# Performance work log

Measured on AMD Instinct MI355X. Metric: run time of the kernel, lower is better.

The kernel has to match this reference:

```python
import jax, jax.numpy as jnp
import numpy as np

N_SAMPLES = 32768; WINDOW = 512; STEP = 256; N_FRAMES = 128
N_COEFFS = 257; N_ATOMS = 32; MODEL_DIM = 128
DILATIONS = (1, 3, 9, 27, 81, 243, 1)


def _conv1d(x, w, b=None, dilation=1, padding=0):
    o = jax.lax.conv_general_dilated(x, w, (1,), [(padding, padding)],
                                     rhs_dilation=(dilation,),
                                     dimension_numbers=('NCH', 'OIH', 'NCH'))
    return o if b is None else o + b[None, :, None]


def _leaky(x):
    return jnp.where(x >= 0, x, 0.2 * x)


def _lin_stack(x, ws, bs, ow, ob):
    # LinearOutputStack: hidden linears with leaky relu, final linear
    for i in range(ws.shape[0]):
        x = _leaky(x @ ws[i].T + bs[i])
    return x @ ow.T + ob


def _conv_up(z, lw, lb, cw, cb, fw, fb_):
    x = (z @ lw.T + lb).reshape(-1, MODEL_DIM, 8)
    for i in range(cw.shape[0]):
        x = jnp.repeat(x, 2, axis=-1)
        x = _leaky(_conv1d(x, cw[i], cb[i], padding=1))
    return _conv1d(x, fw, fb_, padding=1)


def _lin_upsample(x, out_len):
    # F.upsample(mode='linear', align_corners=False)
    L = x.shape[-1]
    src = jnp.clip((jnp.arange(out_len) + 0.5) * (L / out_len) - 0.5, 0.0, L - 1)
    i0 = jnp.floor(src).astype(jnp.int32)
    i1 = jnp.minimum(i0 + 1, L - 1)
    t = (src - i0).astype(x.dtype)
    return x[..., i0] * (1 - t) + x[..., i1] * t


def _generate_event(envelope, transfer, impulse_tf, impulse_noise):
    # envelope [N,1,S], transfer [N,257,2,128], impulse_tf [N,257,2]
    tf = jax.lax.complex(transfer[:, :, 0, :], transfer[:, :, 1, :])  # [N,257,128]
    itf = jax.lax.complex(impulse_tf[..., 0], impulse_tf[..., 1])     # [N,257]
    spec = jnp.fft.rfft(impulse_noise, norm='ortho') * itf
    impulse = jnp.fft.irfft(spec, n=WINDOW, norm='ortho')             # [N,512]
    env = jnp.pad(envelope[:, 0, :], ((0, 0), (0, STEP)))             # pad last frame
    win_idx = (jnp.arange(N_FRAMES) * STEP)[:, None] + jnp.arange(WINDOW)  # [128,512]
    env_frames = env[:, win_idx]                                      # [N,128,512]
    ham = (0.54 - 0.46 * jnp.cos(2 * jnp.pi * jnp.arange(WINDOW) / WINDOW)).astype(envelope.dtype)

    def step(carry, inp):
        env_f, tf_f = inp                      # [N,512], [N,257]
        nxt = impulse * env_f + carry
        s = jnp.fft.rfft(nxt, norm='ortho') * tf_f
        out = jnp.fft.irfft(s, n=WINDOW, norm='ortho') * ham
        return out, out

    _, frames = jax.lax.scan(step, jnp.zeros_like(impulse),
                             (env_frames.transpose(1, 0, 2), tf.transpose(2, 0, 1)))
    frames = frames.transpose(1, 0, 2)         # [N,128,512]
    buf = jnp.zeros((frames.shape[0], N_FRAMES * STEP + STEP), frames.dtype)
    buf = buf.at[:, win_idx].add(frames)       # overlap-add, hop 256
    return buf[:, :N_SAMPLES]


def reference(x, fb_w,
              db_scale_w, db_scale_b, db_gate_w, db_gate_b,
              db_out_w, db_out_b, db_next_w, db_next_b,
              env_lin_w, env_lin_b, env_conv_w, env_conv_b, env_fin_w, env_fin_b,
              tf_lin_w, tf_lin_b, tf_conv_w, tf_conv_b, tf_fin_w, tf_fin_b,
              imp_w, imp_b, imp_out_w, imp_out_b,
              room_w, room_b, room_out_w, room_out_b,
              mix_w, mix_b, mix_out_w, mix_out_b,
              rooms, impulse_noise):
    B = x.shape[0]
    # FilterBank: conv over raw audio, same length
    n = jax.lax.conv_general_dilated(x, fb_w, (1,), [(256, 255)],
                                     dimension_numbers=('NCH', 'OIH', 'NCH'))  # [B,128,S]
    acc = jnp.zeros_like(n)
    for i, d in enumerate(DILATIONS):
        skip = n
        s = _conv1d(n, db_scale_w[i], db_scale_b[i], dilation=d, padding=d)
        g = _conv1d(n, db_gate_w[i], db_gate_b[i], dilation=d, padding=d)
        h = jnp.tanh(s) * jax.nn.sigmoid(g)
        acc = acc + jnp.einsum('oc,bct->bot', db_out_w[i], h) + db_out_b[i][None, :, None]
        n = jnp.einsum('oc,bct->bot', db_next_w[i], h) + db_next_b[i][None, :, None] + skip
    xf = acc                                                   # [B,128,S]
    norms = jnp.linalg.norm(xf, axis=1)                        # [B,S]
    values, indices = jax.lax.top_k(norms, N_ATOMS)            # [B,32]
    latents = jnp.take_along_axis(xf, indices[:, None, :], axis=2)  # [B,128,32]
    latents = latents.transpose(0, 2, 1).reshape(B * N_ATOMS, MODEL_DIM)
    # EventGenerator
    env = _conv_up(latents, env_lin_w, env_lin_b, env_conv_w, env_conv_b, env_fin_w, env_fin_b) ** 2
    env = _lin_upsample(env, N_SAMPLES)                        # [N,1,S]
    transfer = _conv_up(latents, tf_lin_w, tf_lin_b, tf_conv_w, tf_conv_b, tf_fin_w, tf_fin_b)
    transfer = transfer.reshape(-1, N_COEFFS, 2, N_FRAMES)
    impulse_tf = _lin_stack(latents, imp_w, imp_b, imp_out_w, imp_out_b).reshape(-1, N_COEFFS, 2)
    atoms = _generate_event(env, transfer, impulse_tf, impulse_noise).reshape(B, N_ATOMS, N_SAMPLES)
    # scatter-add atoms at topk offsets into 2*S buffer
    pos = indices[:, :, None] + jnp.arange(N_SAMPLES)[None, None, :]   # [B,32,S]
    weighted = atoms * values[:, :, None]

    def scat(pos_b, w_b):
        return jnp.zeros(2 * N_SAMPLES, w_b.dtype).at[pos_b.reshape(-1)].add(w_b.reshape(-1))

    final = jax.vmap(scat)(pos, weighted)[:, None, :N_SAMPLES]         # [B,1,S]
    # reverb mix
    agg = jnp.max(xf, axis=-1)                                         # [B,128]
    r = _lin_stack(agg, room_w, room_b, room_out_w, room_out_b)        # [B,n_rooms]
    m = _lin_stack(agg, mix_w, mix_b, mix_out_w, mix_out_b).reshape(-1, 1, 1)
    ir = jax.nn.softmax(r, axis=-1) @ rooms                            # [B,S]
    fs = jnp.fft.rfft(final[:, 0, :], n=2 * N_SAMPLES)
    irs = jnp.fft.rfft(ir, n=2 * N_SAMPLES)
    wet = jnp.fft.irfft(fs * irs, n=2 * N_SAMPLES)[:, None, :N_SAMPLES]
    return m * wet + final * (1 - m)


def setup_inputs() -> dict:
    key = jax.random.key(0)
    ks = iter(jax.random.split(key, 64))

    def w(*shape, s=0.05):
        return jax.random.normal(next(ks), shape, dtype=jnp.float32) * s

    return {
        'x': jax.random.normal(next(ks), (4, 1, N_SAMPLES), dtype=jnp.float32),
        'fb_w': w(128, 1, 512),
        'db_scale_w': w(7, 128, 128, 3), 'db_scale_b': w(7, 128),
        'db_gate_w': w(7, 128, 128, 3), 'db_gate_b': w(7, 128),
        'db_out_w': w(7, 128, 128), 'db_out_b': w(7, 128),
        'db_next_w': w(7, 128, 128), 'db_next_b': w(7, 128),
        'env_lin_w': w(1024, 128), 'env_lin_b': w(1024),
        'env_conv_w': w(4, 128, 128, 3), 'env_conv_b': w(4, 128),
        'env_fin_w': w(1, 128, 3), 'env_fin_b': w(1),
        'tf_lin_w': w(1024, 128), 'tf_lin_b': w(1024),
        'tf_conv_w': w(4, 128, 128, 3), 'tf_conv_b': w(4, 128),
        'tf_fin_w': w(514, 128, 3), 'tf_fin_b': w(514),
        'imp_w': w(3, 128, 128), 'imp_b': w(3, 128),
        'imp_out_w': w(514, 128), 'imp_out_b': w(514),
        'room_w': w(3, 128, 128), 'room_b': w(3, 128),
        'room_out_w': w(8, 128), 'room_out_b': w(8),
        'mix_w': w(3, 128, 128), 'mix_b': w(3, 128),
        'mix_out_w': w(1, 128), 'mix_out_b': w(1),
        'rooms': w(8, N_SAMPLES, s=0.1),
        'impulse_noise': jax.random.uniform(next(ks), (1, WINDOW), minval=-1.0, maxval=1.0, dtype=jnp.float32),
    }
```

## Files before the change

### kernel.cpp

```cpp
#include <hip/hip_runtime.h>
#include <math.h>

#define NS 32768

static __device__ __forceinline__ float leakyf(float x){ return x >= 0.f ? x : 0.2f*x; }

__global__ void k_wtrans(const float* __restrict__ ws, const float* __restrict__ wg, float* __restrict__ wT)
{
    int idx = blockIdx.x*256 + threadIdx.x;
    const int total = 7*2*3*128*128;
    if (idx >= total) return;
    int o  = idx & 127;
    int cc = (idx >> 7) & 127;
    int j  = (idx >> 14) % 3;
    int sg = (idx / 49152) & 1;
    int l  = idx / 98304;
    const float* src = sg ? wg : ws;
    wT[idx] = src[((l*128 + o)*128 + cc)*3 + j];
}

__global__ void k_wtrans2(const float* __restrict__ wo, const float* __restrict__ wn,
                          float* __restrict__ woT, float* __restrict__ wnT)
{
    int idx = blockIdx.x*256 + threadIdx.x;
    if (idx >= 7*128*128) return;
    int o = idx & 127;
    int c = (idx >> 7) & 127;
    int l = idx >> 14;
    woT[idx] = wo[(l*128 + o)*128 + c];
    wnT[idx] = wn[(l*128 + o)*128 + c];
}

__global__ void k_wtrans_up(const float* __restrict__ ecw, const float* __restrict__ tcw,
                            const float* __restrict__ tfw, float* __restrict__ wtu, float* __restrict__ wtf)
{
    int idx = blockIdx.x*256 + threadIdx.x;
    if (idx < 393216) {
        int o = idx & 127;
        int j = (idx >> 7) % 3;
        int c = (idx / 384) & 127;
        int ml = idx / 49152;
        const float* src = (ml < 4 ? ecw : tcw) + (ml & 3)*49152;
        wtu[idx] = src[(o*128 + c)*3 + j];
    }
    if (idx < 208896) {
        int ct = idx % 544;
        int j = (idx / 544) % 3;
        int c = idx / 1632;
        wtf[idx] = (ct < 514) ? tfw[(ct*128 + c)*3 + j] : 0.f;
    }
}

__global__ __launch_bounds__(512) void k_front(const float* __restrict__ x, const float* __restrict__ fbw,
                                               float* __restrict__ n0)
{
    int b = blockIdx.y;
    int t0 = blockIdx.x * 64;
    int tid = threadIdx.x;
    int t = tid & 63, og = tid >> 6;
    __shared__ float xs[576];
    __shared__ float4 wl[2048];
    for (int i = tid; i < 575; i += 512) {
        int p = t0 + i - 256;
        xs[i] = ((unsigned)p < NS) ? x[b*NS + p] : 0.f;
    }
    float s[16];
    #pragma unroll
    for (int i = 0; i < 16; ++i) s[i] = 0.f;
    for (int kc = 0; kc < 8; ++kc) {
        __syncthreads();
        for (int i = tid; i < 2048; i += 512) {
            int c = i >> 4, k4 = i & 15;
            wl[i] = *(const float4*)(fbw + c*512 + kc*64 + k4*4);
        }
        __syncthreads();
        for (int k4 = 0; k4 < 16; ++k4) {
            int base = t + kc*64 + k4*4;
            float xv0 = xs[base+0], xv1 = xs[base+1], xv2 = xs[base+2], xv3 = xs[base+3];
            #pragma unroll
            for (int i = 0; i < 16; ++i) {
                float4 w = wl[(og*16 + i)*16 + k4];
                s[i] += w.x*xv0 + w.y*xv1 + w.z*xv2 + w.w*xv3;
            }
        }
    }
    #pragma unroll
    for (int i = 0; i < 16; ++i)
        n0[(size_t)(b*128 + og*16 + i)*NS + t0 + t] = s[i];
}

__global__ __launch_bounds__(512) void k_layer(const float* __restrict__ nin, float* __restrict__ nout,
        float* __restrict__ acc, const float* __restrict__ wTl,
        const float* __restrict__ bs, const float* __restrict__ bg,
        const float* __restrict__ woTl, const float* __restrict__ bo,
        const float* __restrict__ wnTl, const float* __restrict__ bn,
        int d, int first)
{
    __shared__ float pool[20480];
    int b = blockIdx.y;
    int t0 = blockIdx.x * 128;
    int tid = threadIdx.x;
    int l = tid & 63, wg = tid >> 6;
    int o0 = wg * 16;
    const float* nb = nin + (size_t)b*128*NS;
    const float4* wq = (const float4*)wTl;

    int sci = tid >> 5;
    int st4 = (tid & 31) * 4;
    int wsgA = 0,              wccA = (tid >> 5) & 15,        wo4A = tid & 31;
    int wsgB = (tid+512) >> 9, wccB = ((tid+512) >> 5) & 15,  wo4B = (tid+512) & 31;

    float4 sreg, wr0, wr1;
    {
        int p = t0 + st4 - d;
        const float* bp = nb + (size_t)sci*NS;
        float v0 = ((unsigned)(p+0) < NS) ? bp[p+0] : 0.f;
        float v1 = ((unsigned)(p+1) < NS) ? bp[p+1] : 0.f;
        float v2 = ((unsigned)(p+2) < NS) ? bp[p+2] : 0.f;
        float v3 = ((unsigned)(p+3) < NS) ? bp[p+3] : 0.f;
        sreg = make_float4(v0,v1,v2,v3);
        wr0 = wq[((wsgA*3 + 0)*128 + wccA)*32 + wo4A];
        wr1 = wq[((wsgB*3 + 0)*128 + wccB)*32 + wo4B];
    }

    float s0[16], s1[16], g0[16], g1[16];
    #pragma unroll
    for (int i = 0; i < 16; ++i) { float bv = bs[o0+i], gv = bg[o0+i]; s0[i]=bv; s1[i]=bv; g0[i]=gv; g1[i]=gv; }

    #pragma unroll 1
    for (int cnt = 0; cnt < 24; ++cnt) {
        int cur = cnt & 1;
        ((float4*)(pool + cur*2048))[tid] = sreg;
        {
            float4* wb = (float4*)(pool + 4096 + cur*4096);
            wb[tid] = wr0; wb[tid + 512] = wr1;
        }
        if (cnt < 23) {
            int nxt = cnt + 1;
            int jn = nxt >> 3, cbn = nxt & 7;
            int p = t0 + st4 + (jn-1)*d;
            const float* bp = nb + (size_t)(cbn*16 + sci)*NS;
            float v0 = ((unsigned)(p+0) < NS) ? bp[p+0] : 0.f;
            float v1 = ((unsigned)(p+1) < NS) ? bp[p+1] : 0.f;
            float v2 = ((unsigned)(p+2) < NS) ? bp[p+2] : 0.f;
            float v3 = ((unsigned)(p+3) < NS) ? bp[p+3] : 0.f;
            sreg = make_float4(v0,v1,v2,v3);
            wr0 = wq[((wsgA*3 + jn)*128 + cbn*16 + wccA)*32 + wo4A];
            wr1 = wq[((wsgB*3 + jn)*128 + cbn*16 + wccB)*32 + wo4B];
        }
        __syncthreads();
        const float* sb = pool + cur*2048;
        const float4* wS = (const float4*)(pool + 4096 + cur*4096);
        const float4* wG = wS + 512;
        for (int ccx = 0; ccx < 16; ++ccx) {
            float nv0 = sb[ccx*128 + l];
            float nv1 = sb[ccx*128 + 64 + l];
            const float4* a4p = wS + ccx*32 + wg*4;
            const float4* b4p = wG + ccx*32 + wg*4;
            #pragma unroll
            for (int i4 = 0; i4 < 4; ++i4) {
                float4 a4 = a4p[i4], b4 = b4p[i4];
                s0[i4*4+0] += nv0*a4.x; s0[i4*4+1] += nv0*a4.y; s0[i4*4+2] += nv0*a4.z; s0[i4*4+3] += nv0*a4.w;
                s1[i4*4+0] += nv1*a4.x; s1[i4*4+1] += nv1*a4.y; s1[i4*4+2] += nv1*a4.z; s1[i4*4+3] += nv1*a4.w;
                g0[i4*4+0] += nv0*b4.x; g0[i4*4+1] += nv0*b4.y; g0[i4*4+2] += nv0*b4.z; g0[i4*4+3] += nv0*b4.w;
                g1[i4*4+0] += nv1*b4.x; g1[i4*4+1] += nv1*b4.y; g1[i4*4+2] += nv1*b4.z; g1[i4*4+3] += nv1*b4.w;
            }
        }
    }

    float hv0[16], hv1[16];
    #pragma unroll
    for (int i = 0; i < 16; ++i) {
        hv0[i] = tanhf(s0[i]) * (1.f/(1.f + __expf(-g0[i])));
        hv1[i] = tanhf(s1[i]) * (1.f/(1.f + __expf(-g1[i])));
    }
    __syncthreads();
    #pragma unroll
    for (int i = 0; i < 16; ++i) {
        pool[(o0+i)*128 + l]      = hv0[i];
        pool[(o0+i)*128 + 64 + l] = hv1[i];
    }

    int aarm = tid >> 8, arest = tid & 255;
    int accx = arest >> 5, ao4 = arest & 31;
    float4 w2r;
    {
        const float4* src = (const float4*)(aarm ? wnTl : woTl);
        w2r = src[(0*8 + accx)*32 + ao4];
    }

    float a0[16], a1[16], n0r[16], n1r[16];
    #pragma unroll
    for (int i = 0; i < 16; ++i) { a0[i]=0.f; a1[i]=0.f; n0r[i]=0.f; n1r[i]=0.f; }

    #pragma unroll 1
    for (int cb2 = 0; cb2 < 16; ++cb2) {
        int cur = cb2 & 1;
        ((float4*)(pool + 16384 + cur*2048))[tid] = w2r;
        if (cb2 < 15) {
            const float4* src = (const float4*)(aarm ? wnTl : woTl);
            w2r = src[((cb2+1)*8 + accx)*32 + ao4];
        }
        __syncthreads();
        const float4* w2S = (const float4*)(pool + 16384 + cur*2048);
        const float4* w2N = w2S + 256;
        for (int ccx = 0; ccx < 8; ++ccx) {
            float h0 = pool[(cb2*8 + ccx)*128 + l];
            float h1 = pool[(cb2*8 + ccx)*128 + 64 + l];
            const float4* wo4p = w2S + ccx*32 + wg*4;
            const float4* wn4p = w2N + ccx*32 + wg*4;
            #pragma unroll
            for (int i4 = 0; i4 < 4; ++i4) {
                float4 w0 = wo4p[i4], w1 = wn4p[i4];
                a0[i4*4+0] += h0*w0.x; a0[i4*4+1] += h0*w0.y; a0[i4*4+2] += h0*w0.z; a0[i4*4+3] += h0*w0.w;
                a1[i4*4+0] += h1*w0.x; a1[i4*4+1] += h1*w0.y; a1[i4*4+2] += h1*w0.z; a1[i4*4+3] += h1*w0.w;
                n0r[i4*4+0] += h0*w1.x; n0r[i4*4+1] += h0*w1.y; n0r[i4*4+2] += h0*w1.z; n0r[i4*4+3] += h0*w1.w;
                n1r[i4*4+0] += h1*w1.x; n1r[i4*4+1] += h1*w1.y; n1r[i4*4+2] += h1*w1.z; n1r[i4*4+3] += h1*w1.w;
            }
        }
    }

    #pragma unroll
    for (int i = 0; i < 16; ++i) {
        int o = o0 + i;
        float bov = bo[o], bnv = bn[o];
        size_t gi0 = (size_t)(b*128 + o)*NS + t0 + l;
        size_t gi1 = gi0 + 64;
        float av0 = first ? 0.f : acc[gi0];
        float av1 = first ? 0.f : acc[gi1];
        acc[gi0] = av0 + a0[i] + bov;
        acc[gi1] = av1 + a1[i] + bov;
        nout[gi0] = n0r[i] + bnv + nin[gi0];
        nout[gi1] = n1r[i] + bnv + nin[gi1];
    }
}

__global__ void k_norms(const float* __restrict__ xf, float* __restrict__ norms)
{
    int b = blockIdx.y;
    int t = blockIdx.x*256 + threadIdx.x;
    float a = 0.f;
    for (int c = 0; c < 128; ++c) {
        float v = xf[(size_t)(b*128 + c)*NS + t];
        a += v*v;
    }
    norms[b*NS + t] = a;
}

__global__ __launch_bounds__(1024) void k_topk(float* __restrict__ norms, float* __restrict__ topv, int* __restrict__ topi)
{
    int b = blockIdx.x;
    int tid = threadIdx.x;
    __shared__ float rv[1024];
    __shared__ int   ri[1024];
    for (int it = 0; it < 32; ++it) {
        float best = -2.f; int bi = 0;
        for (int k = tid; k < NS; k += 1024) {
            float v = norms[b*NS + k];
            if (v > best) { best = v; bi = k; }
        }
        rv[tid] = best; ri[tid] = bi;
        __syncthreads();
        for (int off = 512; off > 0; off >>= 1) {
            if (tid < off) {
                float ov = rv[tid+off]; int oi = ri[tid+off];
                if (ov > rv[tid] || (ov == rv[tid] && oi < ri[tid])) { rv[tid] = ov; ri[tid] = oi; }
            }
            __syncthreads();
        }
        if (tid == 0) {
            topv[b*32 + it] = sqrtf(rv[0]);
            topi[b*32 + it] = ri[0];
            norms[b*NS + ri[0]] = -1.f;
        }
        __syncthreads();
    }
}

__global__ void k_latents(const float* __restrict__ xf, const int* __restrict__ topi, float* __restrict__ lat)
{
    int ev = blockIdx.x; int c = threadIdx.x;
    int b = ev >> 5;
    int idx = topi[ev];
    lat[ev*128 + c] = xf[(size_t)(b*128 + c)*NS + idx];
}

__global__ void k_aggmax(const float* __restrict__ xf, float* __restrict__ agg)
{
    int rc = blockIdx.x;
    int tid = threadIdx.x;
    __shared__ float red[256];
    float m = -3.4e38f;
    const float* row = xf + (size_t)rc*NS;
    for (int t = tid; t < NS; t += 256) m = fmaxf(m, row[t]);
    red[tid] = m; __syncthreads();
    for (int off = 128; off > 0; off >>= 1) {
        if (tid < off) red[tid] = fmaxf(red[tid], red[tid+off]);
        __syncthreads();
    }
    if (tid == 0) agg[rc] = red[0];
}

template<int L2, int NPASS>
__device__ __forceinline__ void up_layerS(const float* __restrict__ wbase, const float* __restrict__ bias,
                                          const float* __restrict__ inb, float* __restrict__ outb,
                                          float* __restrict__ wst, int tid)
{
    constexpr int Lin = L2/2;
    constexpr int OGC = 512/L2;
    constexpr int OR  = 128/NPASS;
    constexpr int NO  = OR/OGC;
    constexpr int LOG = (L2==16)?4:(L2==32)?5:(L2==64)?6:7;
    int p  = tid & (L2-1);
    int og = tid >> LOG;
    int o0 = og*NO;
    #pragma unroll 1
    for (int pass = 0; pass < NPASS; ++pass) {
        int obase = pass*OR;
        float acc[NO];
        #pragma unroll
        for (int k = 0; k < NO; ++k) acc[k] = 0.f;
        #pragma unroll 1
        for (int cc0 = 0; cc0 < 128; cc0 += 16) {
            __syncthreads();
            for (int k = tid; k < 16*3*OR; k += 512) {
                int ci = k / (3*OR); int rem = k - ci*(3*OR);
                int j = rem / OR; int oo = rem - j*OR;
                wst[k] = wbase[(cc0+ci)*384 + j*128 + obase + oo];
            }
            __syncthreads();
            #pragma unroll 1
            for (int ci = 0; ci < 16; ++ci) {
                int c = cc0 + ci;
                float xv[3];
                #pragma unroll
                for (int j = 0; j < 3; ++j) {
                    int iu = p + j - 1;
                    xv[j] = ((unsigned)iu < (unsigned)L2) ? inb[c*Lin + (iu>>1)] : 0.f;
                }
                #pragma unroll
                for (int j = 0; j < 3; ++j) {
                    const float4* w4 = (const float4*)(wst + ci*3*OR + j*OR + o0);
                    #pragma unroll
                    for (int q = 0; q < NO/4; ++q) {
                        float4 w = w4[q];
                        acc[q*4+0] += xv[j]*w.x; acc[q*4+1] += xv[j]*w.y;
                        acc[q*4+2] += xv[j]*w.z; acc[q*4+3] += xv[j]*w.w;
                    }
                }
            }
        }
        #pragma unroll
        for (int k = 0; k < NO; ++k)
            outb[(obase + o0 + k)*L2 + p] = leakyf(acc[k] + bias[obase + o0 + k]);
    }
}

__global__ __launch_bounds__(512) void k_convup3(const float* __restrict__ lat,
    const float* __restrict__ elw, const float* __restrict__ elb, const float* __restrict__ ecb,
    const float* __restrict__ efw, const float* __restrict__ efb,
    const float* __restrict__ tlw, const float* __restrict__ tlb, const float* __restrict__ tcb,
    const float* __restrict__ tfb, const float* __restrict__ wtu, const float* __restrict__ wtf,
    float* __restrict__ envsq, float* __restrict__ tfT)
{
    __shared__ float pool[35008];
    float* latv = pool;
    float* bufA = pool + 128;
    float* bufB = pool + 4288;
    float* bufC = pool + 12480;
    float* wst  = pool + 28864;
    int ev = blockIdx.x;
    int m  = blockIdx.y;
    int tid = threadIdx.x;
    const float* lw = m ? tlw : elw;
    const float* lb = m ? tlb : elb;
    const float* cb = m ? tcb : ecb;
    const float* wu = wtu + m*4*49152;
    if (tid < 128) latv[tid] = lat[ev*128 + tid];
    __syncthreads();
    for (int jj = tid; jj < 1024; jj += 512) {
        float a = lb[jj];
        const float4* w4 = (const float4*)(lw + jj*128);
        #pragma unroll 8
        for (int q = 0; q < 32; ++q) {
            float4 w = w4[q];
            a += w.x*latv[q*4] + w.y*latv[q*4+1] + w.z*latv[q*4+2] + w.w*latv[q*4+3];
        }
        bufA[(jj>>3)*8 + (jj&7)] = a;
    }
    up_layerS<16,1>(wu,        cb,     bufA, bufB, wst, tid);
    up_layerS<32,1>(wu+49152,  cb+128, bufB, bufA, wst, tid);
    up_layerS<64,2>(wu+98304,  cb+256, bufA, bufB, wst, tid);
    up_layerS<128,4>(wu+147456,cb+384, bufB, bufC, wst, tid);
    __syncthreads();
    int p = tid & 127, g = tid >> 7;
    if (m == 0) {
        float s = 0.f;
        #pragma unroll 1
        for (int c = g*32; c < g*32+32; ++c) {
            #pragma unroll
            for (int j = 0; j < 3; ++j) {
                int iu = p + j - 1;
                float xv = ((unsigned)iu < 128u) ? bufC[c*128 + iu] : 0.f;
                s += efw[c*3+j]*xv;
            }
        }
        wst[g*128 + p] = s;
        __syncthreads();
        if (g == 0) {
            float a = wst[p] + wst[128+p] + wst[256+p] + wst[384+p] + efb[0];
            envsq[ev*128 + p] = a*a;
        }
    } else {
        float* trb = bufA;
        #pragma unroll 1
        for (int ctb = 0; ctb < 17; ++ctb) {
            int ct0 = ctb*32;
            float acc[8];
            #pragma unroll
            for (int i = 0; i < 8; ++i) acc[i] = 0.f;
            #pragma unroll 1
            for (int cc0 = 0; cc0 < 128; cc0 += 16) {
                __syncthreads();
                for (int k = tid; k < 1536; k += 512) {
                    int ci = k / 96, rem = k - ci*96;
                    int j = rem >> 5, ctl = rem & 31;
                    wst[k] = wtf[(cc0+ci)*1632 + j*544 + ct0 + ctl];
                }
                __syncthreads();
                #pragma unroll 1
                for (int ci = 0; ci < 16; ++ci) {
                    int c = cc0 + ci;
                    float xv[3];
                    #pragma unroll
                    for (int j = 0; j < 3; ++j) {
                        int iu = p + j - 1;
                        xv[j] = ((unsigned)iu < 128u) ? bufC[c*128 + iu] : 0.f;
                    }
                    #pragma unroll
                    for (int j = 0; j < 3; ++j) {
                        const float4* w4 = (const float4*)(wst + ci*96 + j*32 + g*8);
                        #pragma unroll
                        for (int q = 0; q < 2; ++q) {
                            float4 w = w4[q];
                            acc[q*4+0] += xv[j]*w.x; acc[q*4+1] += xv[j]*w.y;
                            acc[q*4+2] += xv[j]*w.z; acc[q*4+3] += xv[j]*w.w;
                        }
                    }
                }
            }
            __syncthreads();
            #pragma unroll
            for (int i = 0; i < 8; ++i) trb[(g*8 + i)*129 + p] = acc[i];
            __syncthreads();
            int ctl2 = tid & 31, pg = tid >> 5;
            #pragma unroll 1
            for (int ps = 0; ps < 8; ++ps) {
                int pp = ps*16 + pg;
                int ct = ct0 + ctl2;
                if (ct < 514)
                    tfT[(size_t)(ev*128 + pp)*514 + ct] = trb[ctl2*129 + pp] + tfb[ct];
            }
            __syncthreads();
        }
    }
}

__global__ __launch_bounds__(128) void k_itf(const float* __restrict__ lat,
    const float* __restrict__ iw, const float* __restrict__ ib,
    const float* __restrict__ iow, const float* __restrict__ iob,
    float* __restrict__ itf)
{
    int ev = blockIdx.x; int tid = threadIdx.x;
    __shared__ float xa[128], xb[128];
    xa[tid] = lat[ev*128 + tid];
    __syncthreads();
    float* src = xa; float* dst = xb;
    for (int l = 0; l < 3; ++l) {
        float a = ib[l*128 + tid];
        const float* wr = iw + (l*128 + tid)*128;
        for (int k = 0; k < 128; ++k) a += wr[k]*src[k];
        dst[tid] = leakyf(a);
        __syncthreads();
        float* tmp = src; src = dst; dst = tmp;
    }
    for (int o = tid; o < 514; o += 128) {
        float a = iob[o];
        const float* wr = iow + o*128;
        for (int k = 0; k < 128; ++k) a += wr[k]*src[k];
        itf[ev*514 + o] = a;
    }
}

__global__ __launch_bounds__(128) void k_roommix(const float* __restrict__ agg,
    const float* __restrict__ rw, const float* __restrict__ rb,
    const float* __restrict__ row_, const float* __restrict__ rob,
    const float* __restrict__ mw, const float* __restrict__ mb,
    const float* __restrict__ mow, const float* __restrict__ mob,
    float* __restrict__ probs, float* __restrict__ mval)
{
    int b = blockIdx.x; int tid = threadIdx.x;
    __shared__ float xa[128], xb[128], rr[8];
    xa[tid] = agg[b*128 + tid];
    __syncthreads();
    float* src = xa; float* dst = xb;
    for (int l = 0; l < 3; ++l) {
        float a = rb[l*128 + tid];
        const float* wr = rw + (l*128 + tid)*128;
        for (int k = 0; k < 128; ++k) a += wr[k]*src[k];
        dst[tid] = leakyf(a);
        __syncthreads();
        float* tmp = src; src = dst; dst = tmp;
    }
    if (tid < 8) {
        float a = rob[tid];
        const float* wr = row_ + tid*128;
        for (int k = 0; k < 128; ++k) a += wr[k]*src[k];
        rr[tid] = a;
    }
    __syncthreads();
    if (tid == 0) {
        float m = rr[0];
        for (int j = 1; j < 8; ++j) m = fmaxf(m, rr[j]);
        float ssum = 0.f; float e[8];
        for (int j = 0; j < 8; ++j) { e[j] = __expf(rr[j]-m); ssum += e[j]; }
        for (int j = 0; j < 8; ++j) probs[b*8+j] = e[j]/ssum;
    }
    __syncthreads();
    xa[tid] = agg[b*128 + tid];
    __syncthreads();
    src = xa; dst = xb;
    for (int l = 0; l < 3; ++l) {
        float a = mb[l*128 + tid];
        const float* wr = mw + (l*128 + tid)*128;
        for (int k = 0; k < 128; ++k) a += wr[k]*src[k];
        dst[tid] = leakyf(a);
        __syncthreads();
        float* tmp = src; src = dst; dst = tmp;
    }
    if (tid == 0) {
        float a = mob[0];
        for (int k = 0; k < 128; ++k) a += mow[k]*src[k];
        mval[b] = a;
    }
}

__global__ void k_ir(const float* __restrict__ probs, const float* __restrict__ rooms, float* __restrict__ ir)
{
    int b = blockIdx.y;
    int t = blockIdx.x*256 + threadIdx.x;
    float a = 0.f;
    for (int j = 0; j < 8; ++j) a += probs[b*8+j]*rooms[j*NS + t];
    ir[b*NS + t] = a;
}

__device__ __forceinline__ void fft512(float* re, float* im, const float* twr, const float* twi, int tid, bool inverse)
{
    for (int w = tid; w < 512; w += 256) {
        unsigned r = __brev((unsigned)w) >> 23;
        if ((int)r > w) {
            float tr = re[w]; re[w] = re[r]; re[r] = tr;
            float ti = im[w]; im[w] = im[r]; im[r] = ti;
        }
    }
    __syncthreads();
    for (int s = 0; s < 9; ++s) {
        int half = 1 << s;
        int grp = tid >> s;
        int pos = tid & (half-1);
        int i0 = (grp << (s+1)) + pos;
        int i1 = i0 + half;
        int twidx = pos << (8 - s);
        float wr = twr[twidx];
        float wi = inverse ? -twi[twidx] : twi[twidx];
        float r1 = re[i1], q1 = im[i1];
        float tr = wr*r1 - wi*q1;
        float ti = wr*q1 + wi*r1;
        float r0 = re[i0], q0 = im[i0];
        re[i1] = r0 - tr; im[i1] = q0 - ti;
        re[i0] = r0 + tr; im[i0] = q0 + ti;
        __syncthreads();
    }
}

__global__ __launch_bounds__(256) void k_event(const float* __restrict__ tfT, const float* __restrict__ itf,
    const float* __restrict__ envsq, const float* __restrict__ noise, float* __restrict__ atoms)
{
    int ev = blockIdx.x; int tid = threadIdx.x;
    __shared__ float twr[256], twi[256];
    __shared__ float re[512], im[512], carry[512], imp[512], ham[512], acc[256], envl[128];
    if (tid < 128) envl[tid] = envsq[ev*128 + tid];
    {
        float ang = -6.283185307179586f * (float)tid / 512.0f;
        float si, co;
        sincosf(ang, &si, &co);
        twr[tid] = co; twi[tid] = si;
    }
    for (int w = tid; w < 512; w += 256) {
        ham[w] = 0.54f - 0.46f*cosf(6.283185307179586f * (float)w / 512.0f);
        re[w] = noise[w]; im[w] = 0.f; carry[w] = 0.f;
    }
    acc[tid] = 0.f;
    __syncthreads();
    fft512(re, im, twr, twi, tid, false);
    {
        const float* tp = itf + ev*514;
        int k = tid;
        float xr = re[k], xi = im[k];
        float tr = tp[2*k], ti = tp[2*k+1];
        float sr = xr*tr - xi*ti;
        float si = xr*ti + xi*tr;
        if (k == 0) si = 0.f;
        re[k] = sr; im[k] = si;
        if (k >= 1) { re[512-k] = sr; im[512-k] = -si; }
        if (tid == 0) {
            float xr2 = re[256], xi2 = im[256];
            float sr2 = xr2*tp[512] - xi2*tp[513];
            re[256] = sr2; im[256] = 0.f;
        }
    }
    __syncthreads();
    fft512(re, im, twr, twi, tid, true);
    for (int w = tid; w < 512; w += 256) imp[w] = re[w] * (1.0f/512.0f);
    __syncthreads();
    const float inv512 = 1.0f/512.0f;
    for (int f = 0; f < 128; ++f) {
        for (int w = tid; w < 512; w += 256) {
            int tg = f*256 + w;
            float e = 0.f;
            if (tg < NS) {
                float srcp = ((float)tg + 0.5f)*(1.0f/256.0f) - 0.5f;
                srcp = fminf(fmaxf(srcp, 0.f), 127.f);
                int i0 = (int)srcp;
                float fr = srcp - (float)i0;
                int i1 = i0 + 1; if (i1 > 127) i1 = 127;
                e = envl[i0]*(1.f-fr) + envl[i1]*fr;
            }
            re[w] = imp[w]*e + carry[w];
            im[w] = 0.f;
        }
        __syncthreads();
        fft512(re, im, twr, twi, tid, false);
        {
            const float* tp = tfT + ((size_t)ev*128 + f)*514;
            int k = tid;
            float xr = re[k], xi = im[k];
            float tr = tp[2*k], ti = tp[2*k+1];
            float sr = xr*tr - xi*ti;
            float si = xr*ti + xi*tr;
            if (k == 0) si = 0.f;
            re[k] = sr; im[k] = si;
            if (k >= 1) { re[512-k] = sr; im[512-k] = -si; }
            if (tid == 0) {
                float xr2 = re[256], xi2 = im[256];
                float sr2 = xr2*tp[512] - xi2*tp[513];
                re[256] = sr2; im[256] = 0.f;
            }
        }
        __syncthreads();
        fft512(re, im, twr, twi, tid, true);
        float o0 = re[tid]     * inv512 * ham[tid];
        float o1 = re[tid+256] * inv512 * ham[tid+256];
        atoms[(size_t)ev*NS + f*256 + tid] = o0 + acc[tid];
        acc[tid] = o1;
        carry[tid] = o0;
        carry[tid+256] = o1;
        __syncthreads();
    }
}

__global__ void k_gather(const float* __restrict__ atoms, const float* __restrict__ topv,
                         const int* __restrict__ topi, float* __restrict__ fin)
{
    int b = blockIdx.y;
    int t = blockIdx.x*256 + threadIdx.x;
    float s = 0.f;
    for (int a = 0; a < 32; ++a) {
        int ii = topi[b*32 + a];
        if (ii <= t) s += topv[b*32 + a] * atoms[(size_t)(b*32 + a)*NS + (t - ii)];
    }
    fin[b*NS + t] = s;
}

__global__ __launch_bounds__(256) void k_wetpart(const float* __restrict__ fin, const float* __restrict__ ir,
                                                 float* __restrict__ wetp)
{
    int t0 = blockIdx.x*256;
    int by = blockIdx.y;
    int b = by >> 3, cg = by & 7;
    int tid = threadIdx.x;
    __shared__ float fs[256];
    __shared__ float irw[512];
    float wet = 0.f;
    int nch = t0/256 + 1;
    #pragma unroll 1
    for (int q = cg; q < nch; q += 8) {
        int c0 = q*256;
        __syncthreads();
        fs[tid] = fin[b*NS + c0 + tid];
        int dmin = t0 - c0 - 255;
        for (int qq = tid; qq < 511; qq += 256) {
            int dd = dmin + qq;
            irw[qq] = ((unsigned)dd < NS) ? ir[b*NS + dd] : 0.f;
        }
        __syncthreads();
        if (c0 < t0) {
            #pragma unroll 8
            for (int k = 0; k < 256; ++k) wet += fs[k]*irw[tid + 255 - k];
        } else {
            for (int k = 0; k <= tid; ++k) wet += fs[k]*irw[tid + 255 - k];
        }
    }
    wetp[(size_t)by*NS + t0 + tid] = wet;
}

__global__ __launch_bounds__(256) void k_wetsum(const float* __restrict__ fin, const float* __restrict__ wetp,
                                                const float* __restrict__ mval, float* __restrict__ out)
{
    int b = blockIdx.y;
    int t = blockIdx.x*256 + threadIdx.x;
    float w = 0.f;
    #pragma unroll
    for (int cg = 0; cg < 8; ++cg) w += wetp[(size_t)(b*8+cg)*NS + t];
    float m = mval[b];
    float fv = fin[b*NS + t];
    out[b*NS + t] = m*w + fv*(1.f - m);
}

extern "C" void kernel_launch(void* const* d_in, const int* in_sizes, int n_in,
                              void* d_out, int out_size, void* d_ws, size_t ws_size,
                              hipStream_t stream)
{
    (void)in_sizes; (void)n_in; (void)out_size; (void)ws_size;
    const float* x    = (const float*)d_in[0];
    const float* fbw  = (const float*)d_in[1];
    const float* dsw  = (const float*)d_in[2];
    const float* dsb  = (const float*)d_in[3];
    const float* dgw  = (const float*)d_in[4];
    const float* dgb  = (const float*)d_in[5];
    const float* dow  = (const float*)d_in[6];
    const float* dob  = (const float*)d_in[7];
    const float* dnw  = (const float*)d_in[8];
    const float* dnb  = (const float*)d_in[9];
    const float* elw  = (const float*)d_in[10];
    const float* elb  = (const float*)d_in[11];
    const float* ecw  = (const float*)d_in[12];
    const float* ecb  = (const float*)d_in[13];
    const float* efw  = (const float*)d_in[14];
    const float* efb  = (const float*)d_in[15];
    const float* tlw  = (const float*)d_in[16];
    const float* tlb  = (const float*)d_in[17];
    const float* tcw  = (const float*)d_in[18];
    const float* tcb  = (const float*)d_in[19];
    const float* tfw  = (const float*)d_in[20];
    const float* tfb  = (const float*)d_in[21];
    const float* iw   = (const float*)d_in[22];
    const float* ib   = (const float*)d_in[23];
    const float* iow  = (const float*)d_in[24];
    const float* iob  = (const float*)d_in[25];
    const float* rw   = (const float*)d_in[26];
    const float* rb   = (const float*)d_in[27];
    const float* row_ = (const float*)d_in[28];
    const float* rob  = (const float*)d_in[29];
    const float* mw   = (const float*)d_in[30];
    const float* mb   = (const float*)d_in[31];
    const float* mow  = (const float*)d_in[32];
    const float* mob  = (const float*)d_in[33];
    const float* rooms= (const float*)d_in[34];
    const float* noise= (const float*)d_in[35];

    float* ws   = (float*)d_ws;
    float* n0   = ws;
    float* n1   = ws + 16777216;
    float* accb = ws + 33554432;
    float* wT   = ws + 50331648;
    float* woT  = ws + 51707904;
    float* wnT  = ws + 51822592;
    float* envsq= ws + 51937280;
    float* lat  = ws + 51953664;
    float* itfb = ws + 51970048;
    float* norms= ws + 52035840;
    float* topv = ws + 52166912;
    int*   topi = (int*)(ws + 52167040);
    float* agg  = ws + 52167168;
    float* probs= ws + 52167680;
    float* mval = ws + 52167712;
    float* irb  = ws + 52167744;
    float* fin  = ws + 52298816;
    float* tfT  = n0;
    float* atoms= n0 + 8421376;
    float* wetp = n0 + 12615680;
    float* wtu  = n1;
    float* wtf  = n1 + 393216;

    float* out = (float*)d_out;

    k_wtrans<<<dim3((1376256+255)/256), dim3(256), 0, stream>>>(dsw, dgw, wT);
    k_wtrans2<<<dim3((114688+255)/256), dim3(256), 0, stream>>>(dow, dnw, woT, wnT);
    k_front<<<dim3(512,4), dim3(512), 0, stream>>>(x, fbw, n0);

    const int dil[7] = {1,3,9,27,81,243,1};
    float* cin = n0; float* cout = n1;
    for (int l = 0; l < 7; ++l) {
        k_layer<<<dim3(256,4), dim3(512), 0, stream>>>(
            cin, cout, accb, wT + l*98304,
            dsb + l*128, dgb + l*128,
            woT + l*16384, dob + l*128,
            wnT + l*16384, dnb + l*128,
            dil[l], l==0 ? 1 : 0);
        float* tmp = cin; cin = cout; cout = tmp;
    }
    k_norms<<<dim3(128,4), dim3(256), 0, stream>>>(accb, norms);
    k_topk<<<dim3(4), dim3(1024), 0, stream>>>(norms, topv, topi);
    k_latents<<<dim3(128), dim3(128), 0, stream>>>(accb, topi, lat);
    k_aggmax<<<dim3(512), dim3(256), 0, stream>>>(accb, agg);
    k_wtrans_up<<<dim3(1536), dim3(256), 0, stream>>>(ecw, tcw, tfw, wtu, wtf);
    k_convup3<<<dim3(128,2), dim3(512), 0, stream>>>(lat, elw, elb, ecb, efw, efb,
                                                     tlw, tlb, tcb, tfb, wtu, wtf, envsq, tfT);
    k_itf<<<dim3(128), dim3(128), 0, stream>>>(lat, iw, ib, iow, iob, itfb);
    k_roommix<<<dim3(4), dim3(128), 0, stream>>>(agg, rw, rb, row_, rob, mw, mb, mow, mob, probs, mval);
    k_ir<<<dim3(128,4), dim3(256), 0, stream>>>(probs, rooms, irb);
    k_event<<<dim3(128), dim3(256), 0, stream>>>(tfT, itfb, envsq, noise, atoms);
    k_gather<<<dim3(128,4), dim3(256), 0, stream>>>(atoms, topv, topi, fin);
    k_wetpart<<<dim3(128,32), dim3(256), 0, stream>>>(fin, irb, wetp);
    k_wetsum<<<dim3(128,4), dim3(256), 0, stream>>>(fin, wetp, mval, out);
}
```

Before: 5.664 ms.

## Restructure event FFT filtering into DIF/DIT wave-shuffle FFTs with bit-reversed prepacked spectra

Replaces the shared-memory radix-2 FFT pair in the per-event frame loop with a fused forward DIF / inverse DIT transform. Six stages of each transform run in registers through wave shuffles, so the bit-reversal pass and most barriers disappear. The transfer spectra are expanded ahead of time by new prep kernels into full Hermitian float2 arrays in bit-reversed order, so the pointwise multiply needs no reordering. Carry, overlap and the window are kept in registers instead of shared memory. This adds two extra kernel launches and a scratch buffer that reuses existing workspace regions, which risks aliasing with live data.

```diff
diff --git a/kernel.cpp b/kernel.cpp
--- a/kernel.cpp
+++ b/kernel.cpp
@@ -554,118 +554,183 @@
     ir[b*NS + t] = a;
 }
 
-__device__ __forceinline__ void fft512(float* re, float* im, const float* twr, const float* twi, int tid, bool inverse)
-{
-    for (int w = tid; w < 512; w += 256) {
-        unsigned r = __brev((unsigned)w) >> 23;
-        if ((int)r > w) {
-            float tr = re[w]; re[w] = re[r]; re[r] = tr;
-            float ti = im[w]; im[w] = im[r]; im[r] = ti;
-        }
-    }
-    __syncthreads();
-    for (int s = 0; s < 9; ++s) {
-        int half = 1 << s;
-        int grp = tid >> s;
-        int pos = tid & (half-1);
-        int i0 = (grp << (s+1)) + pos;
-        int i1 = i0 + half;
-        int twidx = pos << (8 - s);
-        float wr = twr[twidx];
-        float wi = inverse ? -twi[twidx] : twi[twidx];
-        float r1 = re[i1], q1 = im[i1];
-        float tr = wr*r1 - wi*q1;
-        float ti = wr*q1 + wi*r1;
-        float r0 = re[i0], q0 = im[i0];
-        re[i1] = r0 - tr; im[i1] = q0 - ti;
-        re[i0] = r0 + tr; im[i0] = q0 + ti;
-        __syncthreads();
-    }
-}
-
-__global__ __launch_bounds__(256) void k_event(const float* __restrict__ tfT, const float* __restrict__ itf,
+__global__ void k_tfprep(const float* __restrict__ tfT, float2* __restrict__ Tscr)
+{
+    int f = blockIdx.x, ev = blockIdx.y;
+    const float* tp = tfT + ((size_t)(ev*128 + f))*514;
+    float2* dst = Tscr + ((size_t)(ev*128 + f))*512;
+    int t = threadIdx.x;
+    #pragma unroll
+    for (int h = 0; h < 2; ++h) {
+        int slot = t + h*256;
+        int pos = (int)(__brev((unsigned)slot) >> 23);
+        float2 H;
+        if (pos == 0)        H = make_float2(tp[0], 0.f);
+        else if (pos == 256) H = make_float2(tp[512], 0.f);
+        else if (pos < 256)  H = make_float2(tp[2*pos], tp[2*pos+1]);
+        else { int q = 512 - pos; H = make_float2(tp[2*q], -tp[2*q+1]); }
+        dst[slot] = H;
+    }
+}
+
+__global__ void k_itfprep(const float* __restrict__ itf, float2* __restrict__ iscr)
+{
+    int ev = blockIdx.x;
+    const float* tp = itf + (size_t)ev*514;
+    float2* dst = iscr + (size_t)ev*512;
+    int t = threadIdx.x;
+    #pragma unroll
+    for (int h = 0; h < 2; ++h) {
+        int slot = t + h*256;
+        int pos = (int)(__brev((unsigned)slot) >> 23);
+        float2 H;
+        if (pos == 0)        H = make_float2(tp[0], 0.f);
+        else if (pos == 256) H = make_float2(tp[512], 0.f);
+        else if (pos < 256)  H = make_float2(tp[2*pos], tp[2*pos+1]);
+        else { int q = 512 - pos; H = make_float2(tp[2*q], -tp[2*q+1]); }
+        dst[slot] = H;
+    }
+}
+
+__device__ __forceinline__ void fft_filt(float nx0, float nx1,
+    const float2* __restrict__ Tf,
+    float* __restrict__ re, float* __restrict__ im,
+    const float* __restrict__ twr, const float* __restrict__ twi,
+    int t, float& out0, float& out1)
+{
+    int w = t >> 6, l = t & 63;
+    int c0 = (w << 7) + l;
+    {
+        float d = nx0 - nx1;
+        re[t] = nx0 + nx1; im[t] = 0.f;
+        re[t+256] = d * twr[t]; im[t+256] = d * twi[t];
+    }
+    __syncthreads();
+    {
+        int i = (t & 127) + ((t >> 7) << 8);
+        int j = i & 127;
+        float wr = twr[j*2], wi = twi[j*2];
+        float ur = re[i], ui = im[i], vr = re[i+128], vi = im[i+128];
+        re[i] = ur + vr; im[i] = ui + vi;
+        float dr = ur - vr, di = ui - vi;
+        re[i+128] = dr*wr - di*wi; im[i+128] = dr*wi + di*wr;
+    }
+    __syncthreads();
+    float a0r = re[c0], a0i = im[c0], a1r = re[c0+64], a1i = im[c0+64];
+    {
+        float wr = twr[l*4], wi = twi[l*4];
+        float ur = a0r, ui = a0i;
+        a0r = ur + a1r; a0i = ui + a1i;
+        float dr = ur - a1r, di = ui - a1i;
+        a1r = dr*wr - di*wi; a1i = dr*wi + di*wr;
+    }
+#define DIFS(S, TS) { \
+        int j = l & (S-1); float wr = twr[j*TS], wi = twi[j*TS]; \
+        int up = l & S; \
+        float o0r = __shfl_xor(a0r, S, 64), o0i = __shfl_xor(a0i, S, 64); \
+        float o1r = __shfl_xor(a1r, S, 64), o1i = __shfl_xor(a1i, S, 64); \
+        if (up) { float dr = o0r - a0r, di = o0i - a0i; a0r = dr*wr - di*wi; a0i = dr*wi + di*wr; \
+                  float er = o1r - a1r, ei = o1i - a1i; a1r = er*wr - ei*wi; a1i = er*wi + ei*wr; } \
+        else    { a0r += o0r; a0i += o0i; a1r += o1r; a1i += o1i; } }
+    DIFS(32, 8) DIFS(16, 16) DIFS(8, 32) DIFS(4, 64) DIFS(2, 128) DIFS(1, 256)
+#undef DIFS
+    {
+        float2 T0 = Tf[c0];
+        float2 T1 = Tf[c0+64];
+        float r = a0r*T0.x - a0i*T0.y; a0i = a0r*T0.y + a0i*T0.x; a0r = r;
+        r = a1r*T1.x - a1i*T1.y; a1i = a1r*T1.y + a1i*T1.x; a1r = r;
+    }
+#define DITS(S, TS) { \
+        int j = l & (S-1); float wr = twr[j*TS], wi = -twi[j*TS]; \
+        int up = l & S; \
+        if (up) { float r = a0r*wr - a0i*wi; a0i = a0r*wi + a0i*wr; a0r = r; \
+                  r = a1r*wr - a1i*wi; a1i = a1r*wi + a1i*wr; a1r = r; } \
+        float o0r = __shfl_xor(a0r, S, 64), o0i = __shfl_xor(a0i, S, 64); \
+        float o1r = __shfl_xor(a1r, S, 64), o1i = __shfl_xor(a1i, S, 64); \
+        if (up) { a0r = o0r - a0r; a0i = o0i - a0i; a1r = o1r - a1r; a1i = o1i - a1i; } \
+        else    { a0r += o0r; a0i += o0i; a1r += o1r; a1i += o1i; } }
+    DITS(1, 256) DITS(2, 128) DITS(4, 64) DITS(8, 32) DITS(16, 16) DITS(32, 8)
+#undef DITS
+    {
+        float wr = twr[l*4], wi = -twi[l*4];
+        float vr = a1r*wr - a1i*wi, vi = a1r*wi + a1i*wr;
+        a1r = a0r - vr; a1i = a0i - vi;
+        a0r += vr; a0i += vi;
+    }
+    __syncthreads();
+    re[c0] = a0r; im[c0] = a0i; re[c0+64] = a1r; im[c0+64] = a1i;
+    __syncthreads();
+    {
+        int i = (t & 127) + ((t >> 7) << 8);
+        int j = i & 127;
+        float wr = twr[j*2], wi = -twi[j*2];
+        float ur = re[i], ui = im[i];
+        float br = re[i+128], bi = im[i+128];
+        float vr = br*wr - bi*wi, vi = br*wi + bi*wr;
+        re[i] = ur + vr; im[i] = ui + vi;
+        re[i+128] = ur - vr; im[i+128] = ui - vi;
+    }
+    __syncthreads();
+    {
+        float wr = twr[t], wi = -twi[t];
+        float ur = re[t];
+        float br = re[t+256], bi = im[t+256];
+        float vr = br*wr - bi*wi;
+        out0 = ur + vr;
+        out1 = ur - vr;
+    }
+}
+
+__global__ __launch_bounds__(256) void k_event(const float2* __restrict__ Tscr, const float2* __restrict__ itfscr,
     const float* __restrict__ envsq, const float* __restrict__ noise, float* __restrict__ atoms)
 {
-    int ev = blockIdx.x; int tid = threadIdx.x;
-    __shared__ float twr[256], twi[256];
-    __shared__ float re[512], im[512], carry[512], imp[512], ham[512], acc[256], envl[128];
-    if (tid < 128) envl[tid] = envsq[ev*128 + tid];
-    {
-        float ang = -6.283185307179586f * (float)tid / 512.0f;
+    int ev = blockIdx.x; int t = threadIdx.x;
+    __shared__ float twr[256], twi[256], re[512], im[512], envl[128];
+    if (t < 128) envl[t] = envsq[ev*128 + t];
+    {
+        float ang = -6.283185307179586f * (float)t / 512.0f;
         float si, co;
         sincosf(ang, &si, &co);
-        twr[tid] = co; twi[tid] = si;
-    }
-    for (int w = tid; w < 512; w += 256) {
-        ham[w] = 0.54f - 0.46f*cosf(6.283185307179586f * (float)w / 512.0f);
-        re[w] = noise[w]; im[w] = 0.f; carry[w] = 0.f;
-    }
-    acc[tid] = 0.f;
-    __syncthreads();
-    fft512(re, im, twr, twi, tid, false);
-    {
-        const float* tp = itf + ev*514;
-        int k = tid;
-        float xr = re[k], xi = im[k];
-        float tr = tp[2*k], ti = tp[2*k+1];
-        float sr = xr*tr - xi*ti;
-        float si = xr*ti + xi*tr;
-        if (k == 0) si = 0.f;
-        re[k] = sr; im[k] = si;
-        if (k >= 1) { re[512-k] = sr; im[512-k] = -si; }
-        if (tid == 0) {
-            float xr2 = re[256], xi2 = im[256];
-            float sr2 = xr2*tp[512] - xi2*tp[513];
-            re[256] = sr2; im[256] = 0.f;
-        }
-    }
-    __syncthreads();
-    fft512(re, im, twr, twi, tid, true);
-    for (int w = tid; w < 512; w += 256) imp[w] = re[w] * (1.0f/512.0f);
-    __syncthreads();
-    const float inv512 = 1.0f/512.0f;
+        twr[t] = co; twi[t] = si;
+    }
+    float ham0 = 0.54f - 0.46f*cosf(6.283185307179586f*(float)t/512.0f);
+    float ham1 = 0.54f - 0.46f*cosf(6.283185307179586f*(float)(t+256)/512.0f);
+    __syncthreads();
+    float imp0, imp1;
+    fft_filt(noise[t], noise[t+256], itfscr + (size_t)ev*512, re, im, twr, twi, t, imp0, imp1);
+    const float inv512 = 1.f/512.f;
+    imp0 *= inv512; imp1 *= inv512;
+    float carry0 = 0.f, carry1 = 0.f, accv = 0.f;
+    #pragma unroll 1
     for (int f = 0; f < 128; ++f) {
-        for (int w = tid; w < 512; w += 256) {
-            int tg = f*256 + w;
-            float e = 0.f;
+        float e0, e1;
+        {
+            int tg = f*256 + t;
+            float srcp = ((float)tg + 0.5f)*(1.0f/256.0f) - 0.5f;
+            srcp = fminf(fmaxf(srcp, 0.f), 127.f);
+            int i0 = (int)srcp; float fr = srcp - (float)i0;
+            int i1 = i0 + 1; if (i1 > 127) i1 = 127;
+            e0 = envl[i0]*(1.f-fr) + envl[i1]*fr;
+        }
+        {
+            int tg = f*256 + 256 + t;
+            e1 = 0.f;
             if (tg < NS) {
                 float srcp = ((float)tg + 0.5f)*(1.0f/256.0f) - 0.5f;
                 srcp = fminf(fmaxf(srcp, 0.f), 127.f);
-                int i0 = (int)srcp;
-                float fr = srcp - (float)i0;
+                int i0 = (int)srcp; float fr = srcp - (float)i0;
                 int i1 = i0 + 1; if (i1 > 127) i1 = 127;
-                e = envl[i0]*(1.f-fr) + envl[i1]*fr;
-            }
-            re[w] = imp[w]*e + carry[w];
-            im[w] = 0.f;
-        }
-        __syncthreads();
-        fft512(re, im, twr, twi, tid, false);
-        {
-            const float* tp = tfT + ((size_t)ev*128 + f)*514;
-            int k = tid;
-            float xr = re[k], xi = im[k];
-            float tr = tp[2*k], ti = tp[2*k+1];
-            float sr = xr*tr - xi*ti;
-            float si = xr*ti + xi*tr;
-            if (k == 0) si = 0.f;
-            re[k] = sr; im[k] = si;
-            if (k >= 1) { re[512-k] = sr; im[512-k] = -si; }
-            if (tid == 0) {
-                float xr2 = re[256], xi2 = im[256];
-                float sr2 = xr2*tp[512] - xi2*tp[513];
-                re[256] = sr2; im[256] = 0.f;
-            }
-        }
-        __syncthreads();
-        fft512(re, im, twr, twi, tid, true);
-        float o0 = re[tid]     * inv512 * ham[tid];
-        float o1 = re[tid+256] * inv512 * ham[tid+256];
-        atoms[(size_t)ev*NS + f*256 + tid] = o0 + acc[tid];
-        acc[tid] = o1;
-        carry[tid] = o0;
-        carry[tid+256] = o1;
-        __syncthreads();
+                e1 = envl[i0]*(1.f-fr) + envl[i1]*fr;
+            }
+        }
+        float nx0 = imp0*e0 + carry0;
+        float nx1 = imp1*e1 + carry1;
+        float o0, o1;
+        fft_filt(nx0, nx1, Tscr + ((size_t)(ev*128 + f))*512, re, im, twr, twi, t, o0, o1);
+        o0 *= inv512 * ham0;
+        o1 *= inv512 * ham1;
+        atoms[(size_t)ev*NS + f*256 + t] = o0 + accv;
+        accv = o1; carry0 = o0; carry1 = o1;
     }
 }
 
@@ -792,6 +857,8 @@
     float* wetp = n0 + 12615680;
     float* wtu  = n1;
     float* wtf  = n1 + 393216;
+    float2* Tscr   = (float2*)n1;
+    float2* itfscr = (float2*)accb;
 
     float* out = (float*)d_out;
 
@@ -820,7 +887,9 @@
     k_itf<<<dim3(128), dim3(128), 0, stream>>>(lat, iw, ib, iow, iob, itfb);
     k_roommix<<<dim3(4), dim3(128), 0, stream>>>(agg, rw, rb, row_, rob, mw, mb, mow, mob, probs, mval);
     k_ir<<<dim3(128,4), dim3(256), 0, stream>>>(probs, rooms, irb);
-    k_event<<<dim3(128), dim3(256), 0, stream>>>(tfT, itfb, envsq, noise, atoms);
+    k_tfprep<<<dim3(128,128), dim3(256), 0, stream>>>(tfT, Tscr);
+    k_itfprep<<<dim3(128), dim3(256), 0, stream>>>(itfb, itfscr);
+    k_event<<<dim3(128), dim3(256), 0, stream>>>(Tscr, itfscr, envsq, noise, atoms);
     k_gather<<<dim3(128,4), dim3(256), 0, stream>>>(atoms, topv, topi, fin);
     k_wetpart<<<dim3(128,32), dim3(256), 0, stream>>>(fin, irb, wetp);
     k_wetsum<<<dim3(128,4), dim3(256), 0, stream>>>(fin, wetp, mval, out);
```

Measured after the change: 5.391 ms. -4.8%, faster.
